# Kernel optimization log

Measured on AMD Instinct MI355X. Metric: run time of the kernel, lower is better.

## Reference

```python
import jax, jax.numpy as jnp
import numpy as np

D_MODEL = 1024
N_HEADS = 16
HEAD_DIM = D_MODEL // N_HEADS
HIDDEN = 4096
EPS = 1e-5


def setup_inputs() -> dict:
    key = jax.random.key(0)
    ks = jax.random.split(key, 16)
    s = 1.0 / np.sqrt(D_MODEL)
    sh = 1.0 / np.sqrt(HIDDEN)
    inp = {
        'x': jax.random.normal(ks[0], (4, 2048, D_MODEL), dtype=jnp.float32),
        'Wq': jax.random.normal(ks[1], (D_MODEL, D_MODEL), dtype=jnp.float32) * s,
        'bq': jnp.zeros((D_MODEL,), jnp.float32),
        'Wk': jax.random.normal(ks[2], (D_MODEL, D_MODEL), dtype=jnp.float32) * s,
        'bk': jnp.zeros((D_MODEL,), jnp.float32),
        'Wv': jax.random.normal(ks[3], (D_MODEL, D_MODEL), dtype=jnp.float32) * s,
        'bv': jnp.zeros((D_MODEL,), jnp.float32),
        'Wo': jax.random.normal(ks[4], (D_MODEL, D_MODEL), dtype=jnp.float32) * s,
        'bo': jnp.zeros((D_MODEL,), jnp.float32),
        'gamma1': jnp.ones((D_MODEL,), jnp.float32),
        'beta1': jnp.zeros((D_MODEL,), jnp.float32),
        'W1': jax.random.normal(ks[5], (D_MODEL, HIDDEN), dtype=jnp.float32) * s,
        'b1': jnp.zeros((HIDDEN,), jnp.float32),
        'W2': jax.random.normal(ks[6], (HIDDEN, D_MODEL), dtype=jnp.float32) * sh,
        'b2': jnp.zeros((D_MODEL,), jnp.float32),
        'gamma2': jnp.ones((D_MODEL,), jnp.float32),
        'beta2': jnp.zeros((D_MODEL,), jnp.float32),
    }
    return inp


def _layernorm(x, gamma, beta):
    mu = jnp.mean(x, axis=-1, keepdims=True)
    var = jnp.mean(jnp.square(x - mu), axis=-1, keepdims=True)
    return (x - mu) * jax.lax.rsqrt(var + EPS) * gamma + beta


def _encoder_layer(x, Wq, bq, Wk, bk, Wv, bv, Wo, bo, gamma1, beta1,
                   W1, b1, W2, b2, gamma2, beta2):
    B, S, _ = x.shape
    # projections -> [B, H, S, Dh]
    def split_heads(t):
        return t.reshape(B, S, N_HEADS, HEAD_DIM).transpose(0, 2, 1, 3)
    q = split_heads(x @ Wq + bq)
    k = split_heads(x @ Wk + bk)
    v = split_heads(x @ Wv + bv)
    scale = 1.0 / jnp.sqrt(jnp.float32(HEAD_DIM))
    scores = jnp.einsum('bhqd,bhkd->bhqk', q, k) * scale
    attn = jax.nn.softmax(scores, axis=-1)
    ctx = jnp.einsum('bhqk,bhkd->bhqd', attn, v)
    ctx = ctx.transpose(0, 2, 1, 3).reshape(B, S, D_MODEL)
    attn_out = ctx @ Wo + bo
    # post-norm residual 1
    h = _layernorm(x + attn_out, gamma1, beta1)
    # MLP with exact (erf) GELU, as torch F.gelu default
    mlp = jax.nn.gelu(h @ W1 + b1, approximate=False) @ W2 + b2
    return _layernorm(h + mlp, gamma2, beta2)


def reference(x, Wq, bq, Wk, bk, Wv, bv, Wo, bo, gamma1, beta1,
              W1, b1, W2, b2, gamma2, beta2):
    return _encoder_layer(x, Wq, bq, Wk, bk, Wv, bv, Wo, bo, gamma1, beta1,
                          W1, b1, W2, b2, gamma2, beta2)
```

## Files before the change

kernel.cpp:

```cpp
#include <hip/hip_runtime.h>
#include <cstdint>
#include <cstddef>

using u16 = unsigned short;
using bf16x8 = __attribute__((ext_vector_type(8))) short;
using f32x4  = __attribute__((ext_vector_type(4))) float;

__device__ __forceinline__ u16 f2bf(float f) {
    union { float f; unsigned u; } v; v.f = f;
    unsigned r = v.u + 0x7fffu + ((v.u >> 16) & 1u);
    return (u16)(r >> 16);
}

__device__ __forceinline__ float bf2f(u16 b) {
    union { unsigned u; float f; } v; v.u = (unsigned)b << 16;
    return v.f;
}

__device__ __forceinline__ unsigned cvtpk(float lo, float hi) {
    unsigned r;
    asm("v_cvt_pk_bf16_f32 %0, %1, %2" : "=v"(r) : "v"(lo), "v"(hi));
    return r;
}

__device__ __forceinline__ float fexp2(float x) {
    float r;
    asm("v_exp_f32 %0, %1" : "=v"(r) : "v"(x));
    return r;
}

__device__ __forceinline__ float gelu_f(float x) {
    const float t2 = fminf(x * fmaf(0.10294825f, x * x, 2.3022082f), 80.f);
    const float e  = fexp2(t2);
    return x * e * __frcp_rn(e + 1.0f);
}

__device__ __forceinline__ void gld_lds16(const void* g, void* l) {
    __builtin_amdgcn_global_load_lds(
        (__attribute__((address_space(1))) void*)g,
        (__attribute__((address_space(3))) void*)l, 16, 0, 0);
}

__device__ __forceinline__ f32x4 mfma16(bf16x8 a, bf16x8 b, f32x4 c) {
    return __builtin_amdgcn_mfma_f32_16x16x32_bf16(a, b, c, 0, 0, 0);
}

__global__ __launch_bounds__(256)
void cast_kernel(const float* __restrict__ in, u16* __restrict__ out, int n8) {
    int i = blockIdx.x * 256 + threadIdx.x;
    if (i >= n8) return;
    const float4* p = (const float4*)in;
    float4 a = p[i * 2], b = p[i * 2 + 1];
    ushort4 r0 = make_ushort4(f2bf(a.x), f2bf(a.y), f2bf(a.z), f2bf(a.w));
    ushort4 r1 = make_ushort4(f2bf(b.x), f2bf(b.y), f2bf(b.z), f2bf(b.w));
    ((ushort4*)out)[i * 2]     = r0;
    ((ushort4*)out)[i * 2 + 1] = r1;
}

__global__ __launch_bounds__(256)
void tcast_kernel(const float* __restrict__ in, u16* __restrict__ out, int K, int N,
                  float scale) {
    __shared__ float tile[32][33];
    const int k0 = blockIdx.y * 32, n0 = blockIdx.x * 32;
    const int tx = threadIdx.x & 31, ty = threadIdx.x >> 5;
    #pragma unroll
    for (int r = 0; r < 4; ++r) {
        int k = ty * 4 + r;
        tile[k][tx] = in[(size_t)(k0 + k) * N + n0 + tx];
    }
    __syncthreads();
    #pragma unroll
    for (int r = 0; r < 4; ++r) {
        int n = ty * 4 + r;
        out[(size_t)(n0 + n) * K + k0 + tx] = f2bf(tile[tx][n] * scale);
    }
}

__global__ __launch_bounds__(256)
void bias_concat_kernel(const float* __restrict__ bq, const float* __restrict__ bk,
                        const float* __restrict__ bv, float* __restrict__ out) {
    int i = blockIdx.x * 256 + threadIdx.x;
    if (i >= 3072) return;
    float v;
    if (i < 1024)      v = bq[i] * 0.18033688011112042f;
    else if (i < 2048) v = bk[i - 1024];
    else               v = bv[i - 2048];
    out[i] = v;
}

template <int BM, int EPI>
__global__ __launch_bounds__(512, 1)
void gemm_pipe_kernel(const u16* __restrict__ A, const u16* __restrict__ Bt,
                      const float* __restrict__ bias, void* __restrict__ Cout,
                      int M, int N, int K)
{
    constexpr int AH  = BM * 64;
    constexpr int BH  = 16384;
    constexpr int BUF = 2 * AH + 2 * BH;
    constexpr int LPA = BM / 128;
    constexpr int VMN = LPA + 2;
    constexpr int MR  = BM / 32;
    constexpr int MRH = MR / 2;

    extern __shared__ char smem[];

    const int tid  = threadIdx.x;
    const int wid  = tid >> 6, lane = tid & 63;
    const int l15  = lane & 15, l4 = lane >> 4;
    const int wm   = wid >> 2, wn = wid & 3;

    const int nwg = gridDim.x;
    const int qx = nwg >> 3, rx = nwg & 7;
    const int orig = blockIdx.x;
    const int xcd = orig & 7, jx = orig >> 3;
    const int wgid = (xcd < rx ? xcd * (qx + 1) : rx * (qx + 1) + (xcd - rx) * qx) + jx;
    const int MT = M / BM;
    const int m0 = (wgid % MT) * BM;
    const int n0 = (wgid / MT) * 256;

    const int q0 = tid >> 3, g0 = tid & 7;
    const int u0 = g0 ^ (q0 & 7);
    const int r0 = (q0 << 1) | (u0 >> 2), c80 = u0 & 3;
    const int q1 = q0 + 64;
    const int u1 = g0 ^ (q1 & 7);
    const int r1 = (q1 << 1) | (u1 >> 2), c81 = u1 & 3;
    const u16* aP0 = A  + (size_t)(m0 + r0) * K + c80 * 8;
    const u16* aP1 = A  + (size_t)(m0 + r1) * K + c81 * 8;
    const u16* bP0 = Bt + (size_t)(n0 + r0) * K + c80 * 8;
    const u16* bP1 = Bt + (size_t)(n0 + r1) * K + c81 * 8;
    const int NT = K >> 6;

    auto stageA = [&](int tt, int kk, int nb) {
        char* dst = smem + nb * BUF + kk * AH + tid * 16;
        const int kte = (tt << 6) + (kk << 5);
        gld_lds16(aP0 + kte, dst);
        if constexpr (LPA == 2) gld_lds16(aP1 + kte, dst + 8192);
    };
    auto stageB = [&](int tt, int kk, int nb) {
        char* dst = smem + nb * BUF + 2 * AH + kk * BH + tid * 16;
        const int kte = (tt << 6) + (kk << 5);
        gld_lds16(bP0 + kte, dst);
        gld_lds16(bP1 + kte, dst + 8192);
    };

    auto frag_off = [&](int row) -> int {
        const int q = row >> 1;
        const int u = ((row & 1) << 2) | l4;
        const int g = u ^ (q & 7);
        return q * 128 + g * 16;
    };

    f32x4 acc[MR][4];
    #pragma unroll
    for (int i = 0; i < MR; ++i)
        #pragma unroll
        for (int jj = 0; jj < 4; ++jj) acc[i][jj] = f32x4{0.f, 0.f, 0.f, 0.f};

    stageA(0, 0, 0); stageB(0, 0, 0); stageA(0, 1, 0); stageB(0, 1, 0);
    if constexpr (VMN == 4) asm volatile("s_waitcnt vmcnt(4)" ::: "memory");
    else                    asm volatile("s_waitcnt vmcnt(3)" ::: "memory");
    __builtin_amdgcn_s_barrier();
    asm volatile("" ::: "memory");

    for (int t = 0; t < NT; ++t) {
        const int cur = t & 1, nb = cur ^ 1;
        const int tn = (t + 1 < NT) ? t + 1 : t;
        const char* buf = smem + cur * BUF;
        bf16x8 bfr[4], af[MRH];

        #pragma unroll
        for (int kk = 0; kk < 2; ++kk) {
            #pragma unroll
            for (int fc = 0; fc < 4; ++fc)
                bfr[fc] = *(const bf16x8*)(buf + 2 * AH + kk * BH +
                                           frag_off(wn * 64 + fc * 16 + l15));
            #pragma unroll
            for (int i = 0; i < MRH; ++i)
                af[i] = *(const bf16x8*)(buf + kk * AH +
                                         frag_off(wm * (BM / 2) + i * 16 + l15));
            stageA(tn, kk, nb);
            asm volatile("" ::: "memory");
            __builtin_amdgcn_s_barrier();
            asm volatile("" ::: "memory");
            __builtin_amdgcn_s_setprio(1);
            #pragma unroll
            for (int i = 0; i < MRH; ++i)
                #pragma unroll
                for (int fc = 0; fc < 4; ++fc)
                    acc[i][fc] = mfma16(af[i], bfr[fc], acc[i][fc]);
            __builtin_amdgcn_s_setprio(0);

            #pragma unroll
            for (int i = 0; i < MRH; ++i)
                af[i] = *(const bf16x8*)(buf + kk * AH +
                                         frag_off(wm * (BM / 2) + (MRH + i) * 16 + l15));
            stageB(tn, kk, nb);
            if constexpr (VMN == 4) asm volatile("s_waitcnt vmcnt(4)" ::: "memory");
            else                    asm volatile("s_waitcnt vmcnt(3)" ::: "memory");
            __builtin_amdgcn_s_barrier();
            asm volatile("" ::: "memory");
            __builtin_amdgcn_s_setprio(1);
            #pragma unroll
            for (int i = 0; i < MRH; ++i)
                #pragma unroll
                for (int fc = 0; fc < 4; ++fc)
                    acc[MRH + i][fc] = mfma16(af[i], bfr[fc], acc[MRH + i][fc]);
            __builtin_amdgcn_s_setprio(0);
            asm volatile("" ::: "memory");
        }
    }

    float bv[4];
    #pragma unroll
    for (int fc = 0; fc < 4; ++fc) bv[fc] = bias[n0 + wn * 64 + fc * 16 + l15];
    #pragma unroll
    for (int fr = 0; fr < MR; ++fr) {
        const int rowg = m0 + wm * (BM / 2) + fr * 16 + l4 * 4;
        #pragma unroll
        for (int fc = 0; fc < 4; ++fc) {
            const int colg = n0 + wn * 64 + fc * 16 + l15;
            #pragma unroll
            for (int r = 0; r < 4; ++r) {
                const float v = acc[fr][fc][r] + bv[fc];
                const size_t off = (size_t)(rowg + r) * N + colg;
                if (EPI == 0) ((u16*)Cout)[off] = f2bf(v);
                else          ((u16*)Cout)[off] = f2bf(gelu_f(v));
            }
        }
    }
}

__global__ __launch_bounds__(256)
void vtrans_kernel(const u16* __restrict__ QKV, u16* __restrict__ Vt) {
    __shared__ u16 tile[64][68];
    const int t  = threadIdx.x;
    const int st = blockIdx.x, bh = blockIdx.y;
    const int b  = bh >> 4, h = bh & 15;
    #pragma unroll
    for (int i = 0; i < 2; ++i) {
        int sl = i * 32 + (t >> 3);
        const u16* gp = QKV + ((size_t)b * 2048 + st * 64 + sl) * 3072 + 2048 + h * 64 + (t & 7) * 8;
        ushort4 a = *(const ushort4*)gp;
        ushort4 c = *(const ushort4*)(gp + 4);
        u16* lp = &tile[sl][(t & 7) * 8];
        *(ushort4*)lp       = a;
        *(ushort4*)(lp + 4) = c;
    }
    __syncthreads();
    #pragma unroll
    for (int i = 0; i < 2; ++i) {
        int d  = i * 32 + (t >> 3);
        int s8 = (t & 7) * 8;
        ushort4 o0, o1;
        o0.x = tile[s8 + 0][d]; o0.y = tile[s8 + 1][d]; o0.z = tile[s8 + 2][d]; o0.w = tile[s8 + 3][d];
        o1.x = tile[s8 + 4][d]; o1.y = tile[s8 + 5][d]; o1.z = tile[s8 + 6][d]; o1.w = tile[s8 + 7][d];
        u16* op = Vt + ((size_t)bh * 64 + d) * 2048 + st * 64 + s8;
        *(ushort4*)op       = o0;
        *(ushort4*)(op + 4) = o1;
    }
}

__global__ __launch_bounds__(512)
void attn_kernel(const u16* __restrict__ QKV, const u16* __restrict__ Vt,
                 u16* __restrict__ ctx)
{
    __shared__ u16 smem[24576];

    const int tid = threadIdx.x;
    const int wid = tid >> 6, lane = tid & 63;
    const int l15 = lane & 15, l4 = lane >> 4;
    const int sw  = l15 & 7;
    const int lr  = lane >> 3;
    const int gsrc = ((lane & 7) ^ lr) * 8;
    const int qt = blockIdx.x, bh = blockIdx.y;
    const int b = bh >> 4, h = bh & 15;
    const size_t qrow0 = (size_t)b * 2048 + (size_t)qt * 256;

    u16* const K0 = smem + 16384;
    u16* const V0 = smem + 20480;
    u16* const K1 = smem;
    u16* const V1 = smem + 4096;

    const u16* Qbase = QKV + h * 64;
    const u16* Kbase = QKV + (size_t)b * 2048 * 3072 + 1024 + h * 64;
    const u16* Vbase = Vt + (size_t)bh * 64 * 2048;

    #pragma unroll
    for (int c = 0; c < 4; ++c) {
        const int chunk = wid * 4 + c;
        const int row = chunk * 8 + lr;
        gld_lds16(Qbase + (qrow0 + row) * 3072 + gsrc,
                  (char*)smem + chunk * 1024);
    }

    auto stage_kv = [&](int kt, u16* kb, u16* vb) {
        const int rho = wid * 8 + lr;
        const int krow = (rho & 32) + ((rho & 16) >> 2) + ((rho & 12) << 1) + (rho & 3);
        gld_lds16(Kbase + (size_t)(kt + krow) * 3072 + gsrc,
                  (char*)kb + wid * 1024);
        gld_lds16(Vbase + (size_t)rho * 2048 + kt + gsrc,
                  (char*)vb + wid * 1024);
    };

    stage_kv(0, K0, V0);
    __syncthreads();

    bf16x8 qf[2][2];
    #pragma unroll
    for (int mi = 0; mi < 2; ++mi)
        #pragma unroll
        for (int kk = 0; kk < 2; ++kk)
            qf[mi][kk] = *(const bf16x8*)
                &smem[(size_t)(wid * 32 + mi * 16 + l15) * 64 + (((kk * 4 + l4) ^ sw) * 8)];
    __syncthreads();

    f32x4 accO[2][4] = {};
    f32x4 accL[2] = {};
    const short one_bf = (short)0x3F80;
    const bf16x8 ones = {one_bf, one_bf, one_bf, one_bf,
                         one_bf, one_bf, one_bf, one_bf};

    union U4 { unsigned u[4]; bf16x8 v; };

    auto compute_tile = [&](const u16* kb, const u16* vb) {
        f32x4 st[2][4];
        #pragma unroll
        for (int mi = 0; mi < 2; ++mi)
            #pragma unroll
            for (int ni = 0; ni < 4; ++ni) st[mi][ni] = f32x4{0.f, 0.f, 0.f, 0.f};
        __builtin_amdgcn_s_setprio(1);
        #pragma unroll
        for (int ni = 0; ni < 4; ++ni) {
            bf16x8 kf0 = *(const bf16x8*)&kb[(ni * 16 + l15) * 64 + ((l4 ^ sw) * 8)];
            bf16x8 kf1 = *(const bf16x8*)&kb[(ni * 16 + l15) * 64 + (((4 + l4) ^ sw) * 8)];
            #pragma unroll
            for (int mi = 0; mi < 2; ++mi) {
                st[mi][ni] = mfma16(kf0, qf[mi][0], st[mi][ni]);
                st[mi][ni] = mfma16(kf1, qf[mi][1], st[mi][ni]);
            }
        }
        __builtin_amdgcn_s_setprio(0);

        U4 pb[2][2];
        #pragma unroll
        for (int mi = 0; mi < 2; ++mi) {
            float p[4][4];
            #pragma unroll
            for (int ni = 0; ni < 4; ++ni)
                #pragma unroll
                for (int r = 0; r < 4; ++r)
                    p[ni][r] = fexp2(st[mi][ni][r]);
            #pragma unroll
            for (int ni = 0; ni < 4; ++ni) {
                pb[mi][ni >> 1].u[(ni & 1) * 2 + 0] = cvtpk(p[ni][0], p[ni][1]);
                pb[mi][ni >> 1].u[(ni & 1) * 2 + 1] = cvtpk(p[ni][2], p[ni][3]);
            }
        }

        __builtin_amdgcn_s_setprio(1);
        #pragma unroll
        for (int mi = 0; mi < 2; ++mi) {
            accL[mi] = mfma16(ones, pb[mi][0].v, accL[mi]);
            accL[mi] = mfma16(ones, pb[mi][1].v, accL[mi]);
        }
        #pragma unroll
        for (int di = 0; di < 4; ++di) {
            bf16x8 vf0 = *(const bf16x8*)&vb[(di * 16 + l15) * 64 + ((l4 ^ sw) * 8)];
            bf16x8 vf1 = *(const bf16x8*)&vb[(di * 16 + l15) * 64 + (((4 + l4) ^ sw) * 8)];
            #pragma unroll
            for (int mi = 0; mi < 2; ++mi) {
                accO[mi][di] = mfma16(vf0, pb[mi][0].v, accO[mi][di]);
                accO[mi][di] = mfma16(vf1, pb[mi][1].v, accO[mi][di]);
            }
        }
        __builtin_amdgcn_s_setprio(0);
    };

    for (int it = 0; it < 32; it += 2) {
        if (it + 1 < 32) stage_kv((it + 1) * 64, K1, V1);
        compute_tile(K0, V0);
        __syncthreads();
        if (it + 2 < 32) stage_kv((it + 2) * 64, K0, V0);
        compute_tile(K1, V1);
        __syncthreads();
    }

    #pragma unroll
    for (int mi = 0; mi < 2; ++mi) {
        const float inv = 1.0f / accL[mi][0];
        const size_t q = qrow0 + wid * 32 + mi * 16 + l15;
        #pragma unroll
        for (int di = 0; di < 4; ++di) {
            uint2 w;
            w.x = cvtpk(accO[mi][di][0] * inv, accO[mi][di][1] * inv);
            w.y = cvtpk(accO[mi][di][2] * inv, accO[mi][di][3] * inv);
            *(uint2*)&ctx[q * 1024 + h * 64 + di * 16 + l4 * 4] = w;
        }
    }
}

__global__ __launch_bounds__(256)
void add_ln_kernel(const u16* __restrict__ X, const u16* __restrict__ Y,
                   const float* __restrict__ gamma, const float* __restrict__ beta,
                   float* __restrict__ outf, u16* __restrict__ outb)
{
    const int row = blockIdx.x;
    const int t = threadIdx.x;
    const ushort4 xb = ((const ushort4*)(X + (size_t)row * 1024))[t];
    const ushort4 yb = ((const ushort4*)(Y + (size_t)row * 1024))[t];
    const float v0 = bf2f(xb.x) + bf2f(yb.x);
    const float v1 = bf2f(xb.y) + bf2f(yb.y);
    const float v2 = bf2f(xb.z) + bf2f(yb.z);
    const float v3 = bf2f(xb.w) + bf2f(yb.w);
    float s  = v0 + v1 + v2 + v3;
    float ss = v0 * v0 + v1 * v1 + v2 * v2 + v3 * v3;
    #pragma unroll
    for (int m = 1; m < 64; m <<= 1) {
        s  += __shfl_xor(s, m, 64);
        ss += __shfl_xor(ss, m, 64);
    }
    __shared__ float red[8];
    const int wid = t >> 6, lane = t & 63;
    if (lane == 0) { red[wid] = s; red[4 + wid] = ss; }
    __syncthreads();
    s  = red[0] + red[1] + red[2] + red[3];
    ss = red[4] + red[5] + red[6] + red[7];
    const float mu  = s * (1.f / 1024.f);
    const float var = ss * (1.f / 1024.f) - mu * mu;
    const float inv = rsqrtf(var + 1e-5f);
    const float4 g  = ((const float4*)gamma)[t];
    const float4 bb = ((const float4*)beta)[t];
    float4 o;
    o.x = (v0 - mu) * inv * g.x + bb.x;
    o.y = (v1 - mu) * inv * g.y + bb.y;
    o.z = (v2 - mu) * inv * g.z + bb.z;
    o.w = (v3 - mu) * inv * g.w + bb.w;
    if (outf != nullptr)
        ((float4*)(outf + (size_t)row * 1024))[t] = o;
    if (outb != nullptr) {
        ushort4 ob = make_ushort4(f2bf(o.x), f2bf(o.y), f2bf(o.z), f2bf(o.w));
        ((ushort4*)(outb + (size_t)row * 1024))[t] = ob;
    }
}

extern "C" void kernel_launch(void* const* d_in, const int* in_sizes, int n_in,
                              void* d_out, int out_size, void* d_ws, size_t ws_size,
                              hipStream_t stream)
{
    (void)in_sizes; (void)n_in; (void)out_size; (void)ws_size;
    const float* x   = (const float*)d_in[0];
    const float* Wq  = (const float*)d_in[1];
    const float* bq  = (const float*)d_in[2];
    const float* Wk  = (const float*)d_in[3];
    const float* bk  = (const float*)d_in[4];
    const float* Wv  = (const float*)d_in[5];
    const float* bv  = (const float*)d_in[6];
    const float* Wo  = (const float*)d_in[7];
    const float* bo  = (const float*)d_in[8];
    const float* g1  = (const float*)d_in[9];
    const float* be1 = (const float*)d_in[10];
    const float* W1  = (const float*)d_in[11];
    const float* b1  = (const float*)d_in[12];
    const float* W2  = (const float*)d_in[13];
    const float* b2  = (const float*)d_in[14];
    const float* g2  = (const float*)d_in[15];
    const float* be2 = (const float*)d_in[16];

    constexpr int M = 8192;
    constexpr int D = 1024;
    constexpr int F = 4096;

    char* ws = (char*)d_ws;
    size_t off = 0;
    auto nxt = [&](size_t bytes) -> char* {
        char* p = ws + off;
        off += (bytes + 255) & ~(size_t)255;
        return p;
    };
    u16*   xb    = (u16*)nxt((size_t)M * D * 2);
    u16*   wqkvt = (u16*)nxt((size_t)3 * D * D * 2);
    u16*   wot   = (u16*)nxt((size_t)D * D * 2);
    u16*   w1t   = (u16*)nxt((size_t)F * D * 2);
    u16*   w2t   = (u16*)nxt((size_t)D * F * 2);
    float* bqkv  = (float*)nxt(3072 * 4);
    u16*   qkv   = (u16*)nxt((size_t)M * 3 * D * 2);
    u16*   Vtb   = (u16*)nxt((size_t)M * D * 2);
    u16*   ctx   = (u16*)nxt((size_t)M * D * 2);
    u16*   attn  = (u16*)nxt((size_t)M * D * 2);
    u16*   hb    = (u16*)nxt((size_t)M * D * 2);
    u16*   t1    = qkv;
    u16*   mlp   = attn;

    constexpr float QS = 0.18033688011112042f;
    cast_kernel<<<dim3(M * D / 8 / 256), dim3(256), 0, stream>>>(x, xb, M * D / 8);
    tcast_kernel<<<dim3(D / 32, D / 32), dim3(256), 0, stream>>>(Wq, wqkvt,             D, D, QS);
    tcast_kernel<<<dim3(D / 32, D / 32), dim3(256), 0, stream>>>(Wk, wqkvt + D * D,     D, D, 1.0f);
    tcast_kernel<<<dim3(D / 32, D / 32), dim3(256), 0, stream>>>(Wv, wqkvt + 2 * D * D, D, D, 1.0f);
    tcast_kernel<<<dim3(D / 32, D / 32), dim3(256), 0, stream>>>(Wo, wot, D, D, 1.0f);
    tcast_kernel<<<dim3(F / 32, D / 32), dim3(256), 0, stream>>>(W1, w1t, D, F, 1.0f);
    tcast_kernel<<<dim3(D / 32, F / 32), dim3(256), 0, stream>>>(W2, w2t, F, D, 1.0f);
    bias_concat_kernel<<<dim3(12), dim3(256), 0, stream>>>(bq, bk, bv, bqkv);

    constexpr size_t LDS128 = 2 * (2 * 128 * 64 + 2 * 16384);
    constexpr size_t LDS256 = 2 * (2 * 256 * 64 + 2 * 16384);

    gemm_pipe_kernel<128, 0><<<dim3((M / 128) * (3 * D / 256)), dim3(512), LDS128, stream>>>(
        xb, wqkvt, bqkv, qkv, M, 3 * D, D);

    vtrans_kernel<<<dim3(2048 / 64, 64), dim3(256), 0, stream>>>(qkv, Vtb);
    attn_kernel<<<dim3(2048 / 256, 64), dim3(512), 0, stream>>>(qkv, Vtb, ctx);

    gemm_pipe_kernel<128, 0><<<dim3((M / 128) * (D / 256)), dim3(512), LDS128, stream>>>(
        ctx, wot, bo, attn, M, D, D);
    add_ln_kernel<<<dim3(M), dim3(256), 0, stream>>>(xb, attn, g1, be1, nullptr, hb);

    gemm_pipe_kernel<256, 2><<<dim3((M / 256) * (F / 256)), dim3(512), LDS256, stream>>>(
        hb, w1t, b1, t1, M, F, D);
    gemm_pipe_kernel<128, 0><<<dim3((M / 128) * (D / 256)), dim3(512), LDS128, stream>>>(
        t1, w2t, b2, mlp, M, D, F);
    add_ln_kernel<<<dim3(M), dim3(256), 0, stream>>>(hb, mlp, g2, be2, (float*)d_out, nullptr);
}
```

Before: 391.2 us.

## Merge weight transpose-casts into one launch, add GEMM barriers, remap attention grid

The six per-weight transpose-cast launches become one kernel that picks its source matrix from the block index, removing per-launch overhead and tail gaps. The attention grid is flattened to 1D with a remapping that groups eight heads of one query tile together, likely aimed at better L2/XCD locality. Two extra workgroup barriers are added after each MFMA phase in the pipelined GEMM main loop, likely to keep waves in lockstep or to guard LDS reuse. The added barriers cost synchronisation on every k-step of every GEMM.

```diff
diff --git a/kernel.cpp b/kernel.cpp
--- a/kernel.cpp
+++ b/kernel.cpp
@@ -58,21 +58,36 @@
 }
 
 __global__ __launch_bounds__(256)
-void tcast_kernel(const float* __restrict__ in, u16* __restrict__ out, int K, int N,
-                  float scale) {
+void tcast_all_kernel(const float* __restrict__ Wq, const float* __restrict__ Wk,
+                      const float* __restrict__ Wv, const float* __restrict__ Wo,
+                      const float* __restrict__ W1, const float* __restrict__ W2,
+                      u16* __restrict__ wqkvt, u16* __restrict__ wot,
+                      u16* __restrict__ w1t, u16* __restrict__ w2t)
+{
+    const int g = blockIdx.x;
+    const float* src; u16* dst; int K, N, ti; float scale = 1.0f;
+    if (g < 1024)      { src = Wq; dst = wqkvt;               K = 1024; N = 1024; ti = g;        scale = 0.18033688011112042f; }
+    else if (g < 2048) { src = Wk; dst = wqkvt + 1048576;     K = 1024; N = 1024; ti = g - 1024; }
+    else if (g < 3072) { src = Wv; dst = wqkvt + 2097152;     K = 1024; N = 1024; ti = g - 2048; }
+    else if (g < 4096) { src = Wo; dst = wot;                 K = 1024; N = 1024; ti = g - 3072; }
+    else if (g < 8192) { src = W1; dst = w1t;                 K = 1024; N = 4096; ti = g - 4096; }
+    else               { src = W2; dst = w2t;                 K = 4096; N = 1024; ti = g - 8192; }
+    const int nt = N >> 5;
+    const int bx = ti % nt, by = ti / nt;
+    const int k0 = by * 32, n0 = bx * 32;
+
     __shared__ float tile[32][33];
-    const int k0 = blockIdx.y * 32, n0 = blockIdx.x * 32;
     const int tx = threadIdx.x & 31, ty = threadIdx.x >> 5;
     #pragma unroll
     for (int r = 0; r < 4; ++r) {
         int k = ty * 4 + r;
-        tile[k][tx] = in[(size_t)(k0 + k) * N + n0 + tx];
+        tile[k][tx] = src[(size_t)(k0 + k) * N + n0 + tx];
     }
     __syncthreads();
     #pragma unroll
     for (int r = 0; r < 4; ++r) {
         int n = ty * 4 + r;
-        out[(size_t)(n0 + n) * K + k0 + tx] = f2bf(tile[tx][n] * scale);
+        dst[(size_t)(n0 + n) * K + k0 + tx] = f2bf(tile[tx][n] * scale);
     }
 }
 
@@ -189,6 +204,9 @@
                 for (int fc = 0; fc < 4; ++fc)
                     acc[i][fc] = mfma16(af[i], bfr[fc], acc[i][fc]);
             __builtin_amdgcn_s_setprio(0);
+            asm volatile("" ::: "memory");
+            __builtin_amdgcn_s_barrier();
+            asm volatile("" ::: "memory");
 
             #pragma unroll
             for (int i = 0; i < MRH; ++i)
@@ -206,6 +224,8 @@
                 for (int fc = 0; fc < 4; ++fc)
                     acc[MRH + i][fc] = mfma16(af[i], bfr[fc], acc[MRH + i][fc]);
             __builtin_amdgcn_s_setprio(0);
+            asm volatile("" ::: "memory");
+            __builtin_amdgcn_s_barrier();
             asm volatile("" ::: "memory");
         }
     }
@@ -272,7 +292,9 @@
     const int sw  = l15 & 7;
     const int lr  = lane >> 3;
     const int gsrc = ((lane & 7) ^ lr) * 8;
-    const int qt = blockIdx.x, bh = blockIdx.y;
+    const int g   = blockIdx.x;
+    const int bh  = (g & 7) | ((g >> 6) << 3);
+    const int qt  = (g >> 3) & 7;
     const int b = bh >> 4, h = bh & 15;
     const size_t qrow0 = (size_t)b * 2048 + (size_t)qt * 256;
 
@@ -491,14 +513,9 @@
     u16*   t1    = qkv;
     u16*   mlp   = attn;
 
-    constexpr float QS = 0.18033688011112042f;
     cast_kernel<<<dim3(M * D / 8 / 256), dim3(256), 0, stream>>>(x, xb, M * D / 8);
-    tcast_kernel<<<dim3(D / 32, D / 32), dim3(256), 0, stream>>>(Wq, wqkvt,             D, D, QS);
-    tcast_kernel<<<dim3(D / 32, D / 32), dim3(256), 0, stream>>>(Wk, wqkvt + D * D,     D, D, 1.0f);
-    tcast_kernel<<<dim3(D / 32, D / 32), dim3(256), 0, stream>>>(Wv, wqkvt + 2 * D * D, D, D, 1.0f);
-    tcast_kernel<<<dim3(D / 32, D / 32), dim3(256), 0, stream>>>(Wo, wot, D, D, 1.0f);
-    tcast_kernel<<<dim3(F / 32, D / 32), dim3(256), 0, stream>>>(W1, w1t, D, F, 1.0f);
-    tcast_kernel<<<dim3(D / 32, F / 32), dim3(256), 0, stream>>>(W2, w2t, F, D, 1.0f);
+    tcast_all_kernel<<<dim3(12288), dim3(256), 0, stream>>>(
+        Wq, Wk, Wv, Wo, W1, W2, wqkvt, wot, w1t, w2t);
     bias_concat_kernel<<<dim3(12), dim3(256), 0, stream>>>(bq, bk, bv, bqkv);
 
     constexpr size_t LDS128 = 2 * (2 * 128 * 64 + 2 * 16384);
@@ -508,7 +525,7 @@
         xb, wqkvt, bqkv, qkv, M, 3 * D, D);
 
     vtrans_kernel<<<dim3(2048 / 64, 64), dim3(256), 0, stream>>>(qkv, Vtb);
-    attn_kernel<<<dim3(2048 / 256, 64), dim3(512), 0, stream>>>(qkv, Vtb, ctx);
+    attn_kernel<<<dim3(512), dim3(512), 0, stream>>>(qkv, Vtb, ctx);
 
     gemm_pipe_kernel<128, 0><<<dim3((M / 128) * (D / 256)), dim3(512), LDS128, stream>>>(
         ctx, wot, bo, attn, M, D, D);
```

After: 390.6 us. No clear change (-0.1%).
